# Kernel optimization log

Measured on AMD Instinct MI355X. Metric: run time of the kernel, lower is better.

The kernel has to match this reference:

```python
import jax, jax.numpy as jnp
import numpy as np
from jax import lax

EPS = 1e-5
B, C, H, W = 64, 32, 128, 128

def _bn(x, gamma, beta, mean, var):
    # inference-mode batchnorm over channel dim (NCHW)
    scale = gamma / jnp.sqrt(var + EPS)
    return x * scale[None, :, None, None] + (beta - mean * scale)[None, :, None, None]

def _conv3x3(x, w, b):
    # 3x3 conv, stride 1, padding 1, NCHW / OIHW
    y = lax.conv_general_dilated(x, w, window_strides=(1, 1), padding=((1, 1), (1, 1)),
                                 dimension_numbers=('NCHW', 'OIHW', 'NCHW'))
    return y + b[None, :, None, None]


def setup_inputs() -> dict:
    key = jax.random.key(0)
    ks = jax.random.split(key, 13)
    fan_in = C * 9
    return {
        'x': jax.random.normal(ks[0], (B, C, H, W), jnp.float32),
        'bn1_gamma': jax.random.uniform(ks[1], (C,), jnp.float32, 0.5, 1.5),
        'bn1_beta': jax.random.normal(ks[2], (C,), jnp.float32) * 0.1,
        'bn1_mean': jax.random.normal(ks[3], (C,), jnp.float32) * 0.1,
        'bn1_var': jax.random.uniform(ks[4], (C,), jnp.float32, 0.5, 1.5),
        'w1': jax.random.normal(ks[5], (C, C, 3, 3), jnp.float32) / np.sqrt(fan_in),
        'b1': jax.random.normal(ks[6], (C,), jnp.float32) * 0.01,
        'bn2_gamma': jax.random.uniform(ks[7], (C,), jnp.float32, 0.5, 1.5),
        'bn2_beta': jax.random.normal(ks[8], (C,), jnp.float32) * 0.1,
        'bn2_mean': jax.random.normal(ks[9], (C,), jnp.float32) * 0.1,
        'bn2_var': jax.random.uniform(ks[10], (C,), jnp.float32, 0.5, 1.5),
        'w2': jax.random.normal(ks[11], (C, C, 3, 3), jnp.float32) / np.sqrt(fan_in),
        'b2': jax.random.normal(ks[12], (C,), jnp.float32) * 0.01,
    }


def reference(x, bn1_gamma, bn1_beta, bn1_mean, bn1_var, w1, b1,
              bn2_gamma, bn2_beta, bn2_mean, bn2_var, w2, b2):
    # BN -> ReLU -> conv3x3 -> (dropout: identity in eval) -> BN -> ReLU -> conv3x3
    h = jnp.maximum(_bn(x, bn1_gamma, bn1_beta, bn1_mean, bn1_var), 0.0)
    h = _conv3x3(h, w1, b1)
    h = jnp.maximum(_bn(h, bn2_gamma, bn2_beta, bn2_mean, bn2_var), 0.0)
    h = _conv3x3(h, w2, b2)
    # stride=1 and in_channels==channels -> identity shortcut
    return h + x
```

## Files before the change

### kernel.cpp

```cpp
#include <hip/hip_runtime.h>

#define EPSV 1e-5f

typedef __bf16 bf16x8 __attribute__((ext_vector_type(8)));
typedef float f32x4 __attribute__((ext_vector_type(4)));
typedef float f32x2 __attribute__((ext_vector_type(2)));
typedef unsigned short ushort8 __attribute__((ext_vector_type(8)));

__global__ __launch_bounds__(256) void prep_weights(
    const float* __restrict__ w1, const float* __restrict__ b1,
    const float* __restrict__ g2, const float* __restrict__ be2,
    const float* __restrict__ m2, const float* __restrict__ v2,
    const float* __restrict__ w2,
    const float* __restrict__ g1, const float* __restrict__ be1,
    const float* __restrict__ m1, const float* __restrict__ v1,
    __bf16* __restrict__ wf1, __bf16* __restrict__ wf2,
    float* __restrict__ bias1p, float* __restrict__ sc1, float* __restrict__ sf1) {
  int i = blockIdx.x * 256 + threadIdx.x;
  int conv = i / 9216;
  int rem  = i % 9216;
  int tap  = rem >> 10;
  int r2   = rem & 1023;
  int half = r2 >> 9;
  int lane = (r2 >> 3) & 63;
  int j    = r2 & 7;
  int ci = ((lane >> 4) << 3) + j;
  int co = half * 16 + (lane & 15);
  float val = (conv ? w2 : w1)[(co * 32 + ci) * 9 + tap];
  if (!conv) val *= g2[co] * rsqrtf(v2[co] + EPSV);
  (conv ? wf2 : wf1)[rem] = (__bf16)val;
  if (blockIdx.x == 0 && threadIdx.x < 32) {
    int c = threadIdx.x;
    float s2 = g2[c] * rsqrtf(v2[c] + EPSV);
    bias1p[c] = s2 * b1[c] + (be2[c] - m2[c] * s2);
  }
  if (blockIdx.x == 0 && threadIdx.x >= 64 && threadIdx.x < 96) {
    int c = threadIdx.x - 64;
    float s = g1[c] * rsqrtf(v1[c] + EPSV);
    sc1[c] = s;
    sf1[c] = be1[c] - m1[c] * s;
  }
}

__global__ __launch_bounds__(256, 2) void fused_conv(
    const float* __restrict__ x,
    const float* __restrict__ sc1, const float* __restrict__ sf1,
    const __bf16* __restrict__ wf1, const __bf16* __restrict__ wf2,
    const float* __restrict__ bias1p, const float* __restrict__ b2,
    float* __restrict__ outf) {
  __shared__ __align__(16) unsigned short tile[8 * 4096];
  char* tb = reinterpret_cast<char*>(tile);
  int t = threadIdx.x, lane = t & 63, wv = t >> 6;
  int Bw = blockIdx.x;
  int logical = (Bw & 7) * 256 + (Bw >> 3);
  int b = logical >> 5, h0 = (logical & 31) * 4;

  bf16x8 Bf1[9][2];
  #pragma unroll
  for (int tap = 0; tap < 9; tap++)
    #pragma unroll
    for (int hf = 0; hf < 2; hf++)
      Bf1[tap][hf] = reinterpret_cast<const bf16x8*>(wf1)[(tap * 2 + hf) * 64 + lane];
  float bco1[2] = { bias1p[lane & 15], bias1p[16 + (lane & 15)] };
  float bco2[2] = { b2[lane & 15], b2[16 + (lane & 15)] };

  int cb = lane >> 4;
  int offs[2][3];
  bool bad[2][3];
  #pragma unroll
  for (int g = 0; g < 2; g++)
    #pragma unroll
    for (int dx = 0; dx < 3; dx++) {
      int w = wv * 32 + g * 16 + (lane & 15) + dx - 1;
      bad[g][dx] = (w < 0) || (w > 127);
      int wc = w < 0 ? 0 : (w > 127 ? 127 : w);
      offs[g][dx] = wc * 64 + ((cb ^ ((wc >> 1) & 3)) << 4);
    }

  float sc[8], sf[8];
  #pragma unroll
  for (int cc = 0; cc < 8; cc++) { sc[cc] = sc1[wv * 8 + cc]; sf[cc] = sf1[wv * 8 + cc]; }
  int wb0 = 128 * lane + ((wv ^ (lane & 3)) << 4);
  #pragma unroll
  for (int k = 0; k < 8; k++) {
    int hr = h0 - 2 + k;
    char* dst = tb + k * 8192 + wb0;
    if (hr >= 0 && hr < 128) {
      const float* src = x + (long)(b * 32 + wv * 8) * 16384 + hr * 128 + 2 * lane;
      float p0[8], p1[8];
      #pragma unroll
      for (int cc = 0; cc < 8; cc++) {
        f32x2 v = *reinterpret_cast<const f32x2*>(src + cc * 16384);
        p0[cc] = fmaxf(fmaf(v[0], sc[cc], sf[cc]), 0.0f);
        p1[cc] = fmaxf(fmaf(v[1], sc[cc], sf[cc]), 0.0f);
      }
      bf16x8 a0, a1;
      #pragma unroll
      for (int cc = 0; cc < 8; cc++) { a0[cc] = (__bf16)p0[cc]; a1[cc] = (__bf16)p1[cc]; }
      *reinterpret_cast<bf16x8*>(dst) = a0;
      *reinterpret_cast<bf16x8*>(dst + 64) = a1;
    } else {
      *reinterpret_cast<bf16x8*>(dst) = bf16x8{};
      *reinterpret_cast<bf16x8*>(dst + 64) = bf16x8{};
    }
  }
  __syncthreads();

  f32x4 ha[3][2][2] = {};
  #pragma unroll
  for (int m = -1; m <= 1; m++) {
    if (h0 + m >= 0) {
      #pragma unroll
      for (int dy = 0; dy < 3; dy++) {
        const char* rb = tb + (m + 1 + dy) * 8192;
        #pragma unroll
        for (int dx = 0; dx < 3; dx++)
          #pragma unroll
          for (int g = 0; g < 2; g++) {
            bf16x8 a = *reinterpret_cast<const bf16x8*>(rb + offs[g][dx]);
            if (bad[g][dx]) a = bf16x8{};
            ha[m + 1][g][0] = __builtin_amdgcn_mfma_f32_16x16x32_bf16(a, Bf1[dy * 3 + dx][0], ha[m + 1][g][0], 0, 0, 0);
            ha[m + 1][g][1] = __builtin_amdgcn_mfma_f32_16x16x32_bf16(a, Bf1[dy * 3 + dx][1], ha[m + 1][g][1], 0, 0, 0);
          }
      }
    }
  }
  __syncthreads();
  #pragma unroll
  for (int m = -1; m <= 1; m++) {
    if (h0 + m >= 0) {
      #pragma unroll
      for (int g = 0; g < 2; g++)
        #pragma unroll
        for (int hf = 0; hf < 2; hf++) {
          int co = hf * 16 + (lane & 15);
          #pragma unroll
          for (int j = 0; j < 4; j++) {
            int pix = wv * 32 + g * 16 + ((lane >> 4) << 2) + j;
            float val = fmaxf(ha[m + 1][g][hf][j] + bco1[hf], 0.0f);
            int byte = (m + 1) * 8192 + pix * 64 + (((co >> 3) ^ ((pix >> 1) & 3)) << 4) + (co & 7) * 2;
            *reinterpret_cast<unsigned short*>(tb + byte) =
                __builtin_bit_cast(unsigned short, (__bf16)val);
          }
        }
    } else {
      char* zb = tb + (m + 1) * 8192 + t * 32;
      *reinterpret_cast<ushort8*>(zb) = ushort8{};
      *reinterpret_cast<ushort8*>(zb + 16) = ushort8{};
    }
  }
  __syncthreads();

  #pragma unroll
  for (int r = 0; r < 4; r++) {
    f32x4 c2[2][2] = {};
    #pragma unroll
    for (int dy = 0; dy < 3; dy++) {
      const char* rb = tb + (r + dy) * 8192;
      #pragma unroll
      for (int dx = 0; dx < 3; dx++) {
        bf16x8 B0 = reinterpret_cast<const bf16x8*>(wf2)[((dy * 3 + dx) * 2 + 0) * 64 + lane];
        bf16x8 B1 = reinterpret_cast<const bf16x8*>(wf2)[((dy * 3 + dx) * 2 + 1) * 64 + lane];
        #pragma unroll
        for (int g = 0; g < 2; g++) {
          bf16x8 a = *reinterpret_cast<const bf16x8*>(rb + offs[g][dx]);
          if (bad[g][dx]) a = bf16x8{};
          c2[g][0] = __builtin_amdgcn_mfma_f32_16x16x32_bf16(a, B0, c2[g][0], 0, 0, 0);
          c2[g][1] = __builtin_amdgcn_mfma_f32_16x16x32_bf16(a, B1, c2[g][1], 0, 0, 0);
        }
      }
    }

    if (r < 3) {
      f32x4 hn[2][2] = {};
      bool inimg = (h0 + r + 2) < 128;
      if (inimg) {
        #pragma unroll
        for (int dy = 0; dy < 3; dy++) {
          const char* rb = tb + (r + 3 + dy) * 8192;
          #pragma unroll
          for (int dx = 0; dx < 3; dx++)
            #pragma unroll
            for (int g = 0; g < 2; g++) {
              bf16x8 a = *reinterpret_cast<const bf16x8*>(rb + offs[g][dx]);
              if (bad[g][dx]) a = bf16x8{};
              hn[g][0] = __builtin_amdgcn_mfma_f32_16x16x32_bf16(a, Bf1[dy * 3 + dx][0], hn[g][0], 0, 0, 0);
              hn[g][1] = __builtin_amdgcn_mfma_f32_16x16x32_bf16(a, Bf1[dy * 3 + dx][1], hn[g][1], 0, 0, 0);
            }
        }
      }
      {
        int hr = h0 + r;
        #pragma unroll
        for (int g = 0; g < 2; g++)
          #pragma unroll
          for (int hf = 0; hf < 2; hf++) {
            int co = hf * 16 + (lane & 15);
            int pix0 = wv * 32 + g * 16 + ((lane >> 4) << 2);
            long idx = ((long)(b * 32 + co) * 128 + hr) * 128 + pix0;
            f32x4 xr = *reinterpret_cast<const f32x4*>(x + idx);
            f32x4 o;
            #pragma unroll
            for (int j = 0; j < 4; j++) o[j] = c2[g][hf][j] + bco2[hf] + xr[j];
            *reinterpret_cast<f32x4*>(outf + idx) = o;
          }
      }
      __syncthreads();
      if (inimg) {
        #pragma unroll
        for (int g = 0; g < 2; g++)
          #pragma unroll
          for (int hf = 0; hf < 2; hf++) {
            int co = hf * 16 + (lane & 15);
            #pragma unroll
            for (int j = 0; j < 4; j++) {
              int pix = wv * 32 + g * 16 + ((lane >> 4) << 2) + j;
              float val = fmaxf(hn[g][hf][j] + bco1[hf], 0.0f);
              int byte = (r + 3) * 8192 + pix * 64 + (((co >> 3) ^ ((pix >> 1) & 3)) << 4) + (co & 7) * 2;
              *reinterpret_cast<unsigned short*>(tb + byte) =
                  __builtin_bit_cast(unsigned short, (__bf16)val);
            }
          }
      } else {
        char* zb = tb + (r + 3) * 8192 + t * 32;
        *reinterpret_cast<ushort8*>(zb) = ushort8{};
        *reinterpret_cast<ushort8*>(zb + 16) = ushort8{};
      }
      __syncthreads();
    } else {
      int hr = h0 + r;
      #pragma unroll
      for (int g = 0; g < 2; g++)
        #pragma unroll
        for (int hf = 0; hf < 2; hf++) {
          int co = hf * 16 + (lane & 15);
          int pix0 = wv * 32 + g * 16 + ((lane >> 4) << 2);
          long idx = ((long)(b * 32 + co) * 128 + hr) * 128 + pix0;
          f32x4 xr = *reinterpret_cast<const f32x4*>(x + idx);
          f32x4 o;
          #pragma unroll
          for (int j = 0; j < 4; j++) o[j] = c2[g][hf][j] + bco2[hf] + xr[j];
          *reinterpret_cast<f32x4*>(outf + idx) = o;
        }
    }
  }
}

extern "C" void kernel_launch(void* const* d_in, const int* in_sizes, int n_in,
                              void* d_out, int out_size, void* d_ws, size_t ws_size,
                              hipStream_t stream) {
  const float* x   = (const float*)d_in[0];
  const float* g1  = (const float*)d_in[1];
  const float* be1 = (const float*)d_in[2];
  const float* m1  = (const float*)d_in[3];
  const float* v1  = (const float*)d_in[4];
  const float* w1  = (const float*)d_in[5];
  const float* b1  = (const float*)d_in[6];
  const float* g2  = (const float*)d_in[7];
  const float* be2 = (const float*)d_in[8];
  const float* m2  = (const float*)d_in[9];
  const float* v2  = (const float*)d_in[10];
  const float* w2  = (const float*)d_in[11];
  const float* b2  = (const float*)d_in[12];

  char* ws = (char*)d_ws;
  __bf16* wf1    = (__bf16*)ws;
  __bf16* wf2    = (__bf16*)(ws + 18432);
  float*  bias1p = (float*)(ws + 36864);
  float*  sc1    = (float*)(ws + 36992);
  float*  sf1    = (float*)(ws + 37120);

  prep_weights<<<dim3(72), dim3(256), 0, stream>>>(
      w1, b1, g2, be2, m2, v2, w2, g1, be1, m1, v1, wf1, wf2, bias1p, sc1, sf1);
  fused_conv<<<dim3(2048), dim3(256), 0, stream>>>(
      x, sc1, sf1, wf1, wf2, bias1p, b2, (float*)d_out);
}
```

Measured before the change: 308.1 us.

## Retile fused conv into 6-row by 64-column half-width strips with 8 waves

Replaces the 4-row full-width strip kernel, which used a rolling row pipeline, with a kernel where each 512-thread block handles a 6-row by 64-column tile. The tile carries 8-pixel column halos and 2-row halos. Each of 8 waves computes one intermediate conv1 row (8 rows in total) into shared memory, then the 8 waves split the 24 conv2 row-by-16-pixel tasks three each. This removes the serial per-row sync chain and raises occupancy to 4 blocks per CU with smaller LDS. The cost is more recomputation of conv1 halo rows and columns (8 of 6 rows, 80 of 64 columns) and a ragged last strip.

```diff
diff --git a/kernel.cpp b/kernel.cpp
--- a/kernel.cpp
+++ b/kernel.cpp
@@ -42,18 +42,57 @@
   }
 }
 
-__global__ __launch_bounds__(256, 2) void fused_conv(
+__global__ __launch_bounds__(512, 4) void fused6(
     const float* __restrict__ x,
-    const float* __restrict__ sc1, const float* __restrict__ sf1,
+    const float* __restrict__ sc1v, const float* __restrict__ sf1v,
     const __bf16* __restrict__ wf1, const __bf16* __restrict__ wf2,
     const float* __restrict__ bias1p, const float* __restrict__ b2,
     float* __restrict__ outf) {
-  __shared__ __align__(16) unsigned short tile[8 * 4096];
+  __shared__ __align__(16) unsigned short tile[10 * 2560];
   char* tb = reinterpret_cast<char*>(tile);
   int t = threadIdx.x, lane = t & 63, wv = t >> 6;
-  int Bw = blockIdx.x;
-  int logical = (Bw & 7) * 256 + (Bw >> 3);
-  int b = logical >> 5, h0 = (logical & 31) * 4;
+  int logical = ((blockIdx.x & 7) * 352) + (blockIdx.x >> 3);
+  int half = logical & 1;
+  int sb = logical >> 1;
+  int strip = sb % 22;
+  int b = sb / 22;
+  int h0 = strip * 6;
+  int P0 = half << 6;
+
+  #pragma unroll
+  for (int i = 0; i < 4; i++) {
+    int task = t + 512 * i;
+    if (task < 1600) {
+      int slot = task / 160;
+      int rm = task - slot * 160;
+      int chunk = rm / 40;
+      int pair = rm - chunk * 40;
+      int hr = h0 - 2 + slot;
+      int gpx = P0 - 8 + 2 * pair;
+      char* dst = tb + slot * 5120 + pair * 128 + ((chunk ^ (pair & 3)) << 4);
+      if (hr >= 0 && hr < 128 && gpx >= 0 && gpx <= 126) {
+        const float* src = x + ((long)(b * 32 + chunk * 8) * 128 + hr) * 128 + gpx;
+        f32x4 s0 = *reinterpret_cast<const f32x4*>(sc1v + chunk * 8);
+        f32x4 s1 = *reinterpret_cast<const f32x4*>(sc1v + chunk * 8 + 4);
+        f32x4 f0 = *reinterpret_cast<const f32x4*>(sf1v + chunk * 8);
+        f32x4 f1 = *reinterpret_cast<const f32x4*>(sf1v + chunk * 8 + 4);
+        bf16x8 a0, a1;
+        #pragma unroll
+        for (int cc = 0; cc < 8; cc++) {
+          f32x2 v = *reinterpret_cast<const f32x2*>(src + cc * 16384);
+          float s = cc < 4 ? s0[cc & 3] : s1[cc & 3];
+          float f = cc < 4 ? f0[cc & 3] : f1[cc & 3];
+          a0[cc] = (__bf16)fmaxf(fmaf(v[0], s, f), 0.0f);
+          a1[cc] = (__bf16)fmaxf(fmaf(v[1], s, f), 0.0f);
+        }
+        *reinterpret_cast<bf16x8*>(dst) = a0;
+        *reinterpret_cast<bf16x8*>(dst + 64) = a1;
+      } else {
+        *reinterpret_cast<bf16x8*>(dst) = bf16x8{};
+        *reinterpret_cast<bf16x8*>(dst + 64) = bf16x8{};
+      }
+    }
+  }
 
   bf16x8 Bf1[9][2];
   #pragma unroll
@@ -65,183 +104,98 @@
   float bco2[2] = { b2[lane & 15], b2[16 + (lane & 15)] };
 
   int cb = lane >> 4;
-  int offs[2][3];
-  bool bad[2][3];
-  #pragma unroll
-  for (int g = 0; g < 2; g++)
-    #pragma unroll
-    for (int dx = 0; dx < 3; dx++) {
-      int w = wv * 32 + g * 16 + (lane & 15) + dx - 1;
-      bad[g][dx] = (w < 0) || (w > 127);
-      int wc = w < 0 ? 0 : (w > 127 ? 127 : w);
-      offs[g][dx] = wc * 64 + ((cb ^ ((wc >> 1) & 3)) << 4);
-    }
-
-  float sc[8], sf[8];
-  #pragma unroll
-  for (int cc = 0; cc < 8; cc++) { sc[cc] = sc1[wv * 8 + cc]; sf[cc] = sf1[wv * 8 + cc]; }
-  int wb0 = 128 * lane + ((wv ^ (lane & 3)) << 4);
-  #pragma unroll
-  for (int k = 0; k < 8; k++) {
-    int hr = h0 - 2 + k;
-    char* dst = tb + k * 8192 + wb0;
-    if (hr >= 0 && hr < 128) {
-      const float* src = x + (long)(b * 32 + wv * 8) * 16384 + hr * 128 + 2 * lane;
-      float p0[8], p1[8];
-      #pragma unroll
-      for (int cc = 0; cc < 8; cc++) {
-        f32x2 v = *reinterpret_cast<const f32x2*>(src + cc * 16384);
-        p0[cc] = fmaxf(fmaf(v[0], sc[cc], sf[cc]), 0.0f);
-        p1[cc] = fmaxf(fmaf(v[1], sc[cc], sf[cc]), 0.0f);
-      }
-      bf16x8 a0, a1;
-      #pragma unroll
-      for (int cc = 0; cc < 8; cc++) { a0[cc] = (__bf16)p0[cc]; a1[cc] = (__bf16)p1[cc]; }
-      *reinterpret_cast<bf16x8*>(dst) = a0;
-      *reinterpret_cast<bf16x8*>(dst + 64) = a1;
-    } else {
-      *reinterpret_cast<bf16x8*>(dst) = bf16x8{};
-      *reinterpret_cast<bf16x8*>(dst + 64) = bf16x8{};
-    }
-  }
+  int l15 = lane & 15;
+
   __syncthreads();
 
-  f32x4 ha[3][2][2] = {};
-  #pragma unroll
-  for (int m = -1; m <= 1; m++) {
-    if (h0 + m >= 0) {
-      #pragma unroll
-      for (int dy = 0; dy < 3; dy++) {
-        const char* rb = tb + (m + 1 + dy) * 8192;
-        #pragma unroll
-        for (int dx = 0; dx < 3; dx++)
-          #pragma unroll
-          for (int g = 0; g < 2; g++) {
-            bf16x8 a = *reinterpret_cast<const bf16x8*>(rb + offs[g][dx]);
-            if (bad[g][dx]) a = bf16x8{};
-            ha[m + 1][g][0] = __builtin_amdgcn_mfma_f32_16x16x32_bf16(a, Bf1[dy * 3 + dx][0], ha[m + 1][g][0], 0, 0, 0);
-            ha[m + 1][g][1] = __builtin_amdgcn_mfma_f32_16x16x32_bf16(a, Bf1[dy * 3 + dx][1], ha[m + 1][g][1], 0, 0, 0);
-          }
+  int hrow = h0 + wv - 1;
+  bool hvalid = (hrow >= 0) && (hrow < 128);
+  f32x4 hacc[5][2] = {};
+  if (hvalid) {
+    #pragma unroll
+    for (int dy = 0; dy < 3; dy++) {
+      const char* rb = tb + (wv + dy) * 5120;
+      #pragma unroll
+      for (int dx = 0; dx < 3; dx++) {
+        #pragma unroll
+        for (int g = 0; g < 5; g++) {
+          int lp = g * 16 + l15 + dx - 1;
+          bool bad = (unsigned)lp > 79u;
+          int lpc = bad ? (lp < 0 ? 0 : 79) : lp;
+          int off = lpc * 64 + ((cb ^ ((lpc >> 1) & 3)) << 4);
+          bf16x8 a = *reinterpret_cast<const bf16x8*>(rb + off);
+          if (bad) a = bf16x8{};
+          hacc[g][0] = __builtin_amdgcn_mfma_f32_16x16x32_bf16(a, Bf1[dy * 3 + dx][0], hacc[g][0], 0, 0, 0);
+          hacc[g][1] = __builtin_amdgcn_mfma_f32_16x16x32_bf16(a, Bf1[dy * 3 + dx][1], hacc[g][1], 0, 0, 0);
+        }
       }
     }
   }
   __syncthreads();
-  #pragma unroll
-  for (int m = -1; m <= 1; m++) {
-    if (h0 + m >= 0) {
-      #pragma unroll
-      for (int g = 0; g < 2; g++)
+
+  {
+    char* hslot = tb + wv * 5120;
+    if (hvalid) {
+      #pragma unroll
+      for (int g = 0; g < 5; g++)
         #pragma unroll
         for (int hf = 0; hf < 2; hf++) {
-          int co = hf * 16 + (lane & 15);
+          int co = hf * 16 + l15;
           #pragma unroll
           for (int j = 0; j < 4; j++) {
-            int pix = wv * 32 + g * 16 + ((lane >> 4) << 2) + j;
-            float val = fmaxf(ha[m + 1][g][hf][j] + bco1[hf], 0.0f);
-            int byte = (m + 1) * 8192 + pix * 64 + (((co >> 3) ^ ((pix >> 1) & 3)) << 4) + (co & 7) * 2;
-            *reinterpret_cast<unsigned short*>(tb + byte) =
+            int lp = g * 16 + ((lane >> 4) << 2) + j;
+            float val = fmaxf(hacc[g][hf][j] + bco1[hf], 0.0f);
+            if ((unsigned)(P0 - 8 + lp) >= 128u) val = 0.0f;
+            int byte = lp * 64 + (((co >> 3) ^ ((lp >> 1) & 3)) << 4) + (co & 7) * 2;
+            *reinterpret_cast<unsigned short*>(hslot + byte) =
                 __builtin_bit_cast(unsigned short, (__bf16)val);
           }
         }
     } else {
-      char* zb = tb + (m + 1) * 8192 + t * 32;
-      *reinterpret_cast<ushort8*>(zb) = ushort8{};
-      *reinterpret_cast<ushort8*>(zb + 16) = ushort8{};
+      #pragma unroll
+      for (int q = 0; q < 5; q++)
+        *reinterpret_cast<ushort8*>(hslot + lane * 16 + q * 1024) = ushort8{};
     }
   }
   __syncthreads();
 
   #pragma unroll
-  for (int r = 0; r < 4; r++) {
-    f32x4 c2[2][2] = {};
+  for (int i = 0; i < 3; i++) {
+    int task = wv * 3 + i;
+    int r = task >> 2, g2 = task & 3;
+    int hr = h0 + r;
+    int o2[3];
+    #pragma unroll
+    for (int dx = 0; dx < 3; dx++) {
+      int lp = 8 + g2 * 16 + l15 + dx - 1;
+      o2[dx] = lp * 64 + ((cb ^ ((lp >> 1) & 3)) << 4);
+    }
+    f32x4 c2[2] = {};
     #pragma unroll
     for (int dy = 0; dy < 3; dy++) {
-      const char* rb = tb + (r + dy) * 8192;
+      const char* rb = tb + (r + dy) * 5120;
       #pragma unroll
       for (int dx = 0; dx < 3; dx++) {
-        bf16x8 B0 = reinterpret_cast<const bf16x8*>(wf2)[((dy * 3 + dx) * 2 + 0) * 64 + lane];
-        bf16x8 B1 = reinterpret_cast<const bf16x8*>(wf2)[((dy * 3 + dx) * 2 + 1) * 64 + lane];
-        #pragma unroll
-        for (int g = 0; g < 2; g++) {
-          bf16x8 a = *reinterpret_cast<const bf16x8*>(rb + offs[g][dx]);
-          if (bad[g][dx]) a = bf16x8{};
-          c2[g][0] = __builtin_amdgcn_mfma_f32_16x16x32_bf16(a, B0, c2[g][0], 0, 0, 0);
-          c2[g][1] = __builtin_amdgcn_mfma_f32_16x16x32_bf16(a, B1, c2[g][1], 0, 0, 0);
-        }
-      }
-    }
-
-    if (r < 3) {
-      f32x4 hn[2][2] = {};
-      bool inimg = (h0 + r + 2) < 128;
-      if (inimg) {
-        #pragma unroll
-        for (int dy = 0; dy < 3; dy++) {
-          const char* rb = tb + (r + 3 + dy) * 8192;
-          #pragma unroll
-          for (int dx = 0; dx < 3; dx++)
-            #pragma unroll
-            for (int g = 0; g < 2; g++) {
-              bf16x8 a = *reinterpret_cast<const bf16x8*>(rb + offs[g][dx]);
-              if (bad[g][dx]) a = bf16x8{};
-              hn[g][0] = __builtin_amdgcn_mfma_f32_16x16x32_bf16(a, Bf1[dy * 3 + dx][0], hn[g][0], 0, 0, 0);
-              hn[g][1] = __builtin_amdgcn_mfma_f32_16x16x32_bf16(a, Bf1[dy * 3 + dx][1], hn[g][1], 0, 0, 0);
-            }
-        }
-      }
-      {
-        int hr = h0 + r;
-        #pragma unroll
-        for (int g = 0; g < 2; g++)
-          #pragma unroll
-          for (int hf = 0; hf < 2; hf++) {
-            int co = hf * 16 + (lane & 15);
-            int pix0 = wv * 32 + g * 16 + ((lane >> 4) << 2);
-            long idx = ((long)(b * 32 + co) * 128 + hr) * 128 + pix0;
-            f32x4 xr = *reinterpret_cast<const f32x4*>(x + idx);
-            f32x4 o;
-            #pragma unroll
-            for (int j = 0; j < 4; j++) o[j] = c2[g][hf][j] + bco2[hf] + xr[j];
-            *reinterpret_cast<f32x4*>(outf + idx) = o;
-          }
-      }
-      __syncthreads();
-      if (inimg) {
-        #pragma unroll
-        for (int g = 0; g < 2; g++)
-          #pragma unroll
-          for (int hf = 0; hf < 2; hf++) {
-            int co = hf * 16 + (lane & 15);
-            #pragma unroll
-            for (int j = 0; j < 4; j++) {
-              int pix = wv * 32 + g * 16 + ((lane >> 4) << 2) + j;
-              float val = fmaxf(hn[g][hf][j] + bco1[hf], 0.0f);
-              int byte = (r + 3) * 8192 + pix * 64 + (((co >> 3) ^ ((pix >> 1) & 3)) << 4) + (co & 7) * 2;
-              *reinterpret_cast<unsigned short*>(tb + byte) =
-                  __builtin_bit_cast(unsigned short, (__bf16)val);
-            }
-          }
-      } else {
-        char* zb = tb + (r + 3) * 8192 + t * 32;
-        *reinterpret_cast<ushort8*>(zb) = ushort8{};
-        *reinterpret_cast<ushort8*>(zb + 16) = ushort8{};
-      }
-      __syncthreads();
-    } else {
-      int hr = h0 + r;
-      #pragma unroll
-      for (int g = 0; g < 2; g++)
-        #pragma unroll
-        for (int hf = 0; hf < 2; hf++) {
-          int co = hf * 16 + (lane & 15);
-          int pix0 = wv * 32 + g * 16 + ((lane >> 4) << 2);
-          long idx = ((long)(b * 32 + co) * 128 + hr) * 128 + pix0;
-          f32x4 xr = *reinterpret_cast<const f32x4*>(x + idx);
-          f32x4 o;
-          #pragma unroll
-          for (int j = 0; j < 4; j++) o[j] = c2[g][hf][j] + bco2[hf] + xr[j];
-          *reinterpret_cast<f32x4*>(outf + idx) = o;
-        }
+        int tap = dy * 3 + dx;
+        bf16x8 a = *reinterpret_cast<const bf16x8*>(rb + o2[dx]);
+        bf16x8 B0 = reinterpret_cast<const bf16x8*>(wf2)[(tap * 2 + 0) * 64 + lane];
+        bf16x8 B1 = reinterpret_cast<const bf16x8*>(wf2)[(tap * 2 + 1) * 64 + lane];
+        c2[0] = __builtin_amdgcn_mfma_f32_16x16x32_bf16(a, B0, c2[0], 0, 0, 0);
+        c2[1] = __builtin_amdgcn_mfma_f32_16x16x32_bf16(a, B1, c2[1], 0, 0, 0);
+      }
+    }
+    if (hr < 128) {
+      #pragma unroll
+      for (int hf = 0; hf < 2; hf++) {
+        int co = hf * 16 + l15;
+        int gpx0 = P0 + g2 * 16 + ((lane >> 4) << 2);
+        long idx = ((long)(b * 32 + co) * 128 + hr) * 128 + gpx0;
+        f32x4 xr = *reinterpret_cast<const f32x4*>(x + idx);
+        f32x4 o;
+        #pragma unroll
+        for (int j = 0; j < 4; j++) o[j] = c2[hf][j] + bco2[hf] + xr[j];
+        *reinterpret_cast<f32x4*>(outf + idx) = o;
+      }
     }
   }
 }
@@ -272,6 +226,6 @@
 
   prep_weights<<<dim3(72), dim3(256), 0, stream>>>(
       w1, b1, g2, be2, m2, v2, w2, g1, be1, m1, v1, wf1, wf2, bias1p, sc1, sf1);
-  fused_conv<<<dim3(2048), dim3(256), 0, stream>>>(
+  fused6<<<dim3(2816), dim3(512), 0, stream>>>(
       x, sc1, sf1, wf1, wf2, bias1p, b2, (float*)d_out);
 }
```

Result: slower. 335.8 us (+9.0%).
